# Kernel tuning notes

Measured on AMD Instinct MI355X. Metric: run time of the kernel, lower is better.

Reference implementation:

```python
import jax, jax.numpy as jnp
import numpy as np

B, N, D_IN, D_OUT, R = 8, 2048, 256, 256, 4


def setup_inputs() -> dict:
    key = jax.random.key(0)
    k1, k2, k3, k4 = jax.random.split(key, 4)
    x = jax.random.normal(k1, (B, N, D_IN), dtype=jnp.float32)
    adj = jnp.zeros((1,), dtype=jnp.float32)  # unused by the module
    # relation-type matrix: 0 = no edge, 1..R = relation id
    relation = jax.random.randint(k2, (B, N, N), 0, R + 1, dtype=jnp.int32)
    weight = jax.random.normal(k3, (R, D_IN, D_OUT), dtype=jnp.float32) * 0.05
    bias = jax.random.normal(k4, (D_OUT,), dtype=jnp.float32) * 0.05
    return {"x": x, "adj": adj, "relation": relation, "weight": weight, "bias": bias}


def reference(x, adj, relation, weight, bias):
    # Binary per-relation adjacency masks: [R, B, N, N]
    rel_ids = jnp.arange(1, weight.shape[0] + 1, dtype=relation.dtype)
    masks = (relation[None] == rel_ids[:, None, None, None]).astype(x.dtype)
    # Aggregate neighbors per relation: h[r] = A_r @ x  -> [R, B, N, D_in]
    h = jnp.einsum('rbnm,bmd->rbnd', masks, x)
    # Per-relation output transform, summed over relations: [B, N, D_out]
    y = jnp.einsum('rbnd,rdo->bno', h, weight)
    return y + bias
```

## Files before the change

### kernel.cpp

```cpp
#include <hip/hip_runtime.h>
#include <hip/hip_bf16.h>
#include <stdint.h>

typedef uint32_t u32;
typedef uint64_t u64;
typedef __bf16 bf16x8 __attribute__((ext_vector_type(8)));
typedef float f32x4 __attribute__((ext_vector_type(4)));
typedef u32 u32x4 __attribute__((ext_vector_type(4)));

#define NB 8
#define NN 2048
#define DIN 256
#define DOUT 256
#define NR 4
#define KTOT (NN * NR)

#define XW_BYTES   (NB * DOUT * KTOT * 2)
#define PART_BYTES (NB * NN * DOUT * 4)
#define WT_BYTES   (NR * DIN * DOUT * 2)

__device__ __forceinline__ ushort f2bf(float f) {
  union { float f; u32 u; } c; c.f = f;
  return (ushort)((c.u + 0x7FFFu + ((c.u >> 16) & 1u)) >> 16);
}

__device__ __forceinline__ void gload_lds16(const void* g, void* l) {
  __builtin_amdgcn_global_load_lds(
      (const __attribute__((address_space(1))) u32*)g,
      (__attribute__((address_space(3))) u32*)l, 16, 0, 0);
}

__global__ void k0_wT(const float* __restrict__ w, ushort* __restrict__ wT) {
  int i = blockIdx.x * 256 + threadIdx.x;
  int o = i & 255, d = (i >> 8) & 255, r = i >> 16;
  wT[(r * DOUT + o) * DIN + d] = f2bf(w[i]);
}

__global__ __launch_bounds__(512) void k1_xw(const float* __restrict__ x,
                                             const ushort* __restrict__ wT,
                                             ushort* __restrict__ xwT) {
  __shared__ char smem[65536];
  ushort* As = (ushort*)smem;
  ushort* Bs = (ushort*)(smem + 4096);
  const int t = threadIdx.x, l = t & 63, w = t >> 6;
  const int r = w >> 1, oh = w & 1;
  const int blk = blockIdx.x;
  const int b = blk >> 6, rest = blk & 63, mc = rest >> 1, ot = rest & 1;

  f32x4 acc[4][4] = {};
  const int arow = t >> 3, adc = (t & 7) << 2;
  const float* xg = x + ((size_t)(b * NN + mc * 64 + arow) * DIN + adc);

  for (int s = 0; s < 8; ++s) {
    const int d0 = s * 32;
    float4 xv = *(const float4*)(xg + d0);
    ushort4 a4;
    a4.x = f2bf(xv.x); a4.y = f2bf(xv.y); a4.z = f2bf(xv.z); a4.w = f2bf(xv.w);
    *(ushort4*)(As + arow * 32 + adc) = a4;
#pragma unroll
    for (int i = 0; i < 4; ++i) {
      int off = i * 4096 + t * 8;
      int rr = off >> 12, rem = off & 4095, o = rem >> 5, dd = rem & 31;
      const ushort* src = wT + ((size_t)(rr * DOUT + ot * 128 + o) * DIN + d0 + dd);
      gload_lds16(src, Bs + off);
    }
    __syncthreads();
    bf16x8 af[4];
#pragma unroll
    for (int fm = 0; fm < 4; ++fm)
      af[fm] = *(const bf16x8*)(As + (fm * 16 + (l & 15)) * 32 + (l >> 4) * 8);
#pragma unroll
    for (int fo = 0; fo < 4; ++fo) {
      bf16x8 bf = *(const bf16x8*)(Bs + (size_t)(r * 128 + oh * 64 + fo * 16 + (l & 15)) * 32 + (l >> 4) * 8);
#pragma unroll
      for (int fm = 0; fm < 4; ++fm)
        acc[fm][fo] = __builtin_amdgcn_mfma_f32_16x16x32_bf16(af[fm], bf, acc[fm][fo], 0, 0, 0);
    }
    __syncthreads();
  }
  ushort* Cs = (ushort*)smem;
#pragma unroll
  for (int fm = 0; fm < 4; ++fm)
#pragma unroll
    for (int fo = 0; fo < 4; ++fo)
#pragma unroll
      for (int j = 0; j < 4; ++j) {
        int o_loc = oh * 64 + fo * 16 + (l & 15);
        int ml = fm * 16 + (l >> 4) * 4 + j;
        Cs[o_loc * 256 + ml * 4 + r] = f2bf(acc[fm][fo][j]);
      }
  __syncthreads();
#pragma unroll
  for (int i = 0; i < 8; ++i) {
    int el = (i * 512 + t) * 8;
    int o_loc = el >> 8, kp = el & 255;
    *(uint4*)(xwT + (size_t)(b * DOUT + ot * 128 + o_loc) * KTOT + mc * 256 + kp) =
        *(const uint4*)(Cs + el);
  }
}

__global__ __launch_bounds__(256, 2) void k2_main(const int* __restrict__ rel,
                                                  const ushort* __restrict__ xwT,
                                                  float* __restrict__ out,
                                                  float* __restrict__ part) {
  __shared__ char smem[65536];
  const int t = threadIdx.x, l = t & 63, w = t >> 6;
  const int wr = w >> 1, wc = w & 1;
  const int logical = (blockIdx.x & 7) * 64 + (blockIdx.x >> 3);
  const int b = logical >> 6;
  const int nt = (logical >> 2) & 15;
  const int ks = (logical >> 1) & 1;
  const int ot = logical & 1;

  f32x4 acc[4][4] = {};
  const int arow = t >> 1, half = t & 1;
  const int* relg = rel + ((size_t)(b * NN + nt * 128 + arow) * NN + ks * 1024 + half * 8);
  const ushort* xwb = xwT + (size_t)(b * DOUT + ot * 128) * KTOT + ks * 4096;

  const int kd = (((t & 7) ^ ((t >> 3) & 7)) << 3);
  const int brow = t >> 3;

  const int aswz = (arow & 7) << 4;

#define STAGE_B(sidx, bufoff)                                                  \
  {                                                                            \
    _Pragma("unroll") for (int i = 0; i < 4; ++i) {                            \
      int o = i * 32 + brow;                                                   \
      gload_lds16(xwb + (size_t)o * KTOT + (sidx) * 64 + kd,                   \
                  smem + (bufoff) + i * 4096 + t * 16);                        \
    }                                                                          \
  }

#define EXPAND_A(bufoff, v0, v1)                                               \
  {                                                                            \
    char* rowp = smem + (bufoff) + arow * 128;                                 \
    int vv[8] = {v0.x, v0.y, v0.z, v0.w, v1.x, v1.y, v1.z, v1.w};              \
    _Pragma("unroll") for (int p = 0; p < 4; ++p) {                            \
      int va = vv[2 * p], vb = vv[2 * p + 1];                                  \
      u32 sa = ((u32)(va - 1) & 3u) * 16u;                                     \
      u32 sb = ((u32)(vb - 1) & 3u) * 16u;                                     \
      u64 ha = va ? (0x3F80ull << sa) : 0ull;                                  \
      u64 hb = vb ? (0x3F80ull << sb) : 0ull;                                  \
      u32x4 e = {(u32)ha, (u32)(ha >> 32), (u32)hb, (u32)(hb >> 32)};          \
      *(u32x4*)(rowp + (((half * 64 + p * 16)) ^ aswz)) = e;                   \
    }                                                                          \
  }

  STAGE_B(0, 32768);
  {
    int4 p0 = *(const int4*)(relg);
    int4 p1 = *(const int4*)(relg + 4);
    EXPAND_A(0, p0, p1);
  }
  __syncthreads();

  const int fr = l & 15, fq = l >> 4;
  const int rswz = (fr & 7) << 4;

  for (int s = 0; s < 64; ++s) {
    const int cur = (s & 1) * 16384;
    const int nxt = ((s + 1) & 1) * 16384;
    int4 r0, r1;
    if (s < 63) {
      STAGE_B(s + 1, 32768 + nxt);
      r0 = *(const int4*)(relg + (s + 1) * 16);
      r1 = *(const int4*)(relg + (s + 1) * 16 + 4);
    }
    const char* Ac = smem + cur;
    const char* Bc = smem + 32768 + cur;
#pragma unroll
    for (int kk = 0; kk < 2; ++kk) {
      bf16x8 af[4], bfv[4];
      const int colb = (kk * 64 + fq * 16) ^ rswz;
#pragma unroll
      for (int fm = 0; fm < 4; ++fm)
        af[fm] = *(const bf16x8*)(Ac + (wr * 64 + fm * 16 + fr) * 128 + colb);
#pragma unroll
      for (int fo = 0; fo < 4; ++fo)
        bfv[fo] = *(const bf16x8*)(Bc + (wc * 64 + fo * 16 + fr) * 128 + colb);
#pragma unroll
      for (int fm = 0; fm < 4; ++fm)
#pragma unroll
        for (int fo = 0; fo < 4; ++fo)
          acc[fm][fo] = __builtin_amdgcn_mfma_f32_16x16x32_bf16(af[fm], bfv[fo], acc[fm][fo], 0, 0, 0);
    }
    if (s < 63) EXPAND_A(nxt, r0, r1);
    __syncthreads();
  }

  float* dst = ks ? part : out;
#pragma unroll
  for (int fm = 0; fm < 4; ++fm)
#pragma unroll
    for (int fo = 0; fo < 4; ++fo) {
      int n = nt * 128 + wr * 64 + fm * 16 + fq * 4;
      int o = ot * 128 + wc * 64 + fo * 16 + fr;
#pragma unroll
      for (int j = 0; j < 4; ++j)
        dst[(size_t)(b * NN + n + j) * DOUT + o] = acc[fm][fo][j];
    }
#undef STAGE_B
#undef EXPAND_A
}

__global__ void k3_add(float* __restrict__ out, const float* __restrict__ part,
                       const float* __restrict__ bias) {
  int i = blockIdx.x * 256 + threadIdx.x;
  float4 o = ((const float4*)out)[i];
  float4 p = ((const float4*)part)[i];
  float4 bv = ((const float4*)bias)[i & 63];
  float4 rr;
  rr.x = o.x + p.x + bv.x;
  rr.y = o.y + p.y + bv.y;
  rr.z = o.z + p.z + bv.z;
  rr.w = o.w + p.w + bv.w;
  ((float4*)out)[i] = rr;
}

extern "C" void kernel_launch(void* const* d_in, const int* in_sizes, int n_in,
                              void* d_out, int out_size, void* d_ws, size_t ws_size,
                              hipStream_t stream) {
  const float* x = (const float*)d_in[0];
  const int* rel = (const int*)d_in[2];
  const float* wgt = (const float*)d_in[3];
  const float* bias = (const float*)d_in[4];
  float* out = (float*)d_out;
  char* ws = (char*)d_ws;

  ushort* xwT = (ushort*)ws;
  float* part = (float*)(ws + XW_BYTES);
  ushort* wT = (ushort*)(ws + XW_BYTES + PART_BYTES);

  k0_wT<<<1024, 256, 0, stream>>>(wgt, wT);
  k1_xw<<<512, 512, 0, stream>>>(x, wT, xwT);
  k2_main<<<512, 256, 0, stream>>>(rel, xwT, out, part);
  k3_add<<<4096, 256, 0, stream>>>(out, part, bias);
}
```

Measured before the change: 126.1 us.

## Register-stage B tiles two steps ahead with manual barriers in relation GEMM

The main aggregation kernel no longer uses direct global-to-LDS loads for the xw tile. Each tile is now loaded into registers two k-steps ahead and written to the alternate LDS buffer after the MFMA step. The loop is unrolled by two with named double buffers, and the relation ints are also prefetched two steps ahead. Barriers wait only on LDS counters, and s_setprio raises wave priority around the MFMA block. The aim is to hide global latency with a deeper prefetch, at the cost of more VGPRs and extra LDS write instructions that could hurt the 2-blocks-per-CU occupancy.

```diff
diff --git a/kernel.cpp b/kernel.cpp
--- a/kernel.cpp
+++ b/kernel.cpp
@@ -17,7 +17,6 @@
 
 #define XW_BYTES   (NB * DOUT * KTOT * 2)
 #define PART_BYTES (NB * NN * DOUT * 4)
-#define WT_BYTES   (NR * DIN * DOUT * 2)
 
 __device__ __forceinline__ ushort f2bf(float f) {
   union { float f; u32 u; } c; c.f = f;
@@ -117,24 +116,25 @@
   const int* relg = rel + ((size_t)(b * NN + nt * 128 + arow) * NN + ks * 1024 + half * 8);
   const ushort* xwb = xwT + (size_t)(b * DOUT + ot * 128) * KTOT + ks * 4096;
 
-  const int kd = (((t & 7) ^ ((t >> 3) & 7)) << 3);
+  char* const Ab0 = smem;
+  char* const Ab1 = smem + 16384;
+  char* const Bb0 = smem + 32768;
+  char* const Bb1 = smem + 49152;
+
   const int brow = t >> 3;
-
+  const int bcol = (t & 7) * 8;
+  const int bwcol = ((t & 7) * 16) ^ (((t >> 3) & 7) << 4);
   const int aswz = (arow & 7) << 4;
-
-#define STAGE_B(sidx, bufoff)                                                  \
+  const int fr = l & 15, fq = l >> 4;
+  const int rswz = (fr & 7) << 4;
+
+  uint4 bs0[4], bs1[4];
+  int4 rs0a, rs0b, rs1a, rs1b;
+
+#define EXPAND_A(ABASE, V0, V1)                                                \
   {                                                                            \
-    _Pragma("unroll") for (int i = 0; i < 4; ++i) {                            \
-      int o = i * 32 + brow;                                                   \
-      gload_lds16(xwb + (size_t)o * KTOT + (sidx) * 64 + kd,                   \
-                  smem + (bufoff) + i * 4096 + t * 16);                        \
-    }                                                                          \
-  }
-
-#define EXPAND_A(bufoff, v0, v1)                                               \
-  {                                                                            \
-    char* rowp = smem + (bufoff) + arow * 128;                                 \
-    int vv[8] = {v0.x, v0.y, v0.z, v0.w, v1.x, v1.y, v1.z, v1.w};              \
+    char* rowp = (ABASE) + arow * 128;                                         \
+    int vv[8] = {V0.x, V0.y, V0.z, V0.w, V1.x, V1.y, V1.z, V1.w};              \
     _Pragma("unroll") for (int p = 0; p < 4; ++p) {                            \
       int va = vv[2 * p], vb = vv[2 * p + 1];                                  \
       u32 sa = ((u32)(va - 1) & 3u) * 16u;                                     \
@@ -142,50 +142,67 @@
       u64 ha = va ? (0x3F80ull << sa) : 0ull;                                  \
       u64 hb = vb ? (0x3F80ull << sb) : 0ull;                                  \
       u32x4 e = {(u32)ha, (u32)(ha >> 32), (u32)hb, (u32)(hb >> 32)};          \
-      *(u32x4*)(rowp + (((half * 64 + p * 16)) ^ aswz)) = e;                   \
+      *(u32x4*)(rowp + ((half * 64 + p * 16) ^ aswz)) = e;                     \
     }                                                                          \
   }
 
-  STAGE_B(0, 32768);
-  {
-    int4 p0 = *(const int4*)(relg);
-    int4 p1 = *(const int4*)(relg + 4);
-    EXPAND_A(0, p0, p1);
-  }
-  __syncthreads();
-
-  const int fr = l & 15, fq = l >> 4;
-  const int rswz = (fr & 7) << 4;
-
-  for (int s = 0; s < 64; ++s) {
-    const int cur = (s & 1) * 16384;
-    const int nxt = ((s + 1) & 1) * 16384;
-    int4 r0, r1;
-    if (s < 63) {
-      STAGE_B(s + 1, 32768 + nxt);
-      r0 = *(const int4*)(relg + (s + 1) * 16);
-      r1 = *(const int4*)(relg + (s + 1) * 16 + 4);
-    }
-    const char* Ac = smem + cur;
-    const char* Bc = smem + 32768 + cur;
-#pragma unroll
-    for (int kk = 0; kk < 2; ++kk) {
-      bf16x8 af[4], bfv[4];
-      const int colb = (kk * 64 + fq * 16) ^ rswz;
-#pragma unroll
-      for (int fm = 0; fm < 4; ++fm)
-        af[fm] = *(const bf16x8*)(Ac + (wr * 64 + fm * 16 + fr) * 128 + colb);
-#pragma unroll
-      for (int fo = 0; fo < 4; ++fo)
-        bfv[fo] = *(const bf16x8*)(Bc + (wc * 64 + fo * 16 + fr) * 128 + colb);
-#pragma unroll
-      for (int fm = 0; fm < 4; ++fm)
-#pragma unroll
-        for (int fo = 0; fo < 4; ++fo)
-          acc[fm][fo] = __builtin_amdgcn_mfma_f32_16x16x32_bf16(af[fm], bfv[fo], acc[fm][fo], 0, 0, 0);
-    }
-    if (s < 63) EXPAND_A(nxt, r0, r1);
-    __syncthreads();
+#define LOAD_B(SET, S)                                                         \
+  _Pragma("unroll") for (int i = 0; i < 4; ++i)                                \
+    SET[i] = *(const uint4*)(xwb + (size_t)(brow + 32 * i) * KTOT + (S) * 64 + bcol);
+
+#define WRITE_B(BBASE, SET)                                                    \
+  _Pragma("unroll") for (int i = 0; i < 4; ++i)                                \
+    *(uint4*)((BBASE) + (brow + 32 * i) * 128 + bwcol) = SET[i];
+
+#define BAR()                                                                  \
+  asm volatile("s_waitcnt lgkmcnt(0)" ::: "memory");                           \
+  __builtin_amdgcn_s_barrier();                                                \
+  __builtin_amdgcn_sched_barrier(0);
+
+#define MFMA_STEP(AC, BC)                                                      \
+  __builtin_amdgcn_s_setprio(1);                                               \
+  _Pragma("unroll") for (int kk = 0; kk < 2; ++kk) {                           \
+    bf16x8 af[4], bfv[4];                                                      \
+    const int colb = (kk * 64 + fq * 16) ^ rswz;                               \
+    _Pragma("unroll") for (int fm = 0; fm < 4; ++fm)                           \
+      af[fm] = *(const bf16x8*)((AC) + (wr * 64 + fm * 16 + fr) * 128 + colb); \
+    _Pragma("unroll") for (int fo = 0; fo < 4; ++fo)                           \
+      bfv[fo] = *(const bf16x8*)((BC) + (wc * 64 + fo * 16 + fr) * 128 + colb);\
+    _Pragma("unroll") for (int fm = 0; fm < 4; ++fm)                           \
+      _Pragma("unroll") for (int fo = 0; fo < 4; ++fo)                         \
+        acc[fm][fo] = __builtin_amdgcn_mfma_f32_16x16x32_bf16(                 \
+            af[fm], bfv[fo], acc[fm][fo], 0, 0, 0);                            \
+  }                                                                            \
+  __builtin_amdgcn_s_setprio(0);
+
+#define BODY(S, P, Q)                                                          \
+  {                                                                            \
+    if ((S) < 62) {                                                            \
+      LOAD_B(bs##P, (S) + 2);                                                  \
+      rs##P##a = *(const int4*)(relg + ((S) + 2) * 16);                        \
+      rs##P##b = *(const int4*)(relg + ((S) + 2) * 16 + 4);                    \
+    }                                                                          \
+    MFMA_STEP(Ab##P, Bb##P);                                                   \
+    if ((S) < 63) {                                                            \
+      WRITE_B(Bb##Q, bs##Q);                                                   \
+      EXPAND_A(Ab##Q, rs##Q##a, rs##Q##b);                                     \
+    }                                                                          \
+    BAR();                                                                     \
+  }
+
+  LOAD_B(bs0, 0);
+  rs0a = *(const int4*)(relg);
+  rs0b = *(const int4*)(relg + 4);
+  LOAD_B(bs1, 1);
+  rs1a = *(const int4*)(relg + 16);
+  rs1b = *(const int4*)(relg + 20);
+  WRITE_B(Bb0, bs0);
+  EXPAND_A(Ab0, rs0a, rs0b);
+  BAR();
+
+  for (int s = 0; s < 64; s += 2) {
+    BODY(s, 0, 1);
+    BODY(s + 1, 1, 0);
   }
 
   float* dst = ks ? part : out;
@@ -199,7 +216,11 @@
       for (int j = 0; j < 4; ++j)
         dst[(size_t)(b * NN + n + j) * DOUT + o] = acc[fm][fo][j];
     }
-#undef STAGE_B
+#undef BODY
+#undef MFMA_STEP
+#undef BAR
+#undef WRITE_B
+#undef LOAD_B
 #undef EXPAND_A
 }
 
```

Result: slower. 185.9 us (+47.4%).
